# Kernel optimization log

Hardware: AMD Instinct MI355X
Metric: run time of the kernel (lower is better)

The kernel has to match this reference:

```python
import jax, jax.numpy as jnp
import numpy as np


def avg_pool_2x2(x):
    # x: [B, H, W, C] -> [B, H//2, W//2, C], non-overlapping 2x2 mean (Keras AveragePooling2D default)
    B, H, W, C = x.shape
    return x.reshape(B, H // 2, 2, W // 2, 2, C).mean(axis=(2, 4))


def setup_inputs() -> dict:
    key = jax.random.key(0)
    k1, k2, k3, k4, k5 = jax.random.split(key, 5)
    B, H, W, C = 16, 64, 64, 512
    x = jax.random.normal(k1, (B, H, W, C), dtype=jnp.float32)
    Wf = jax.random.normal(k2, (C, C // 8), dtype=jnp.float32) * 0.02
    Wg = jax.random.normal(k3, (C, C // 8), dtype=jnp.float32) * 0.02
    Wh = jax.random.normal(k4, (C, C // 2), dtype=jnp.float32) * 0.02
    Wo = jax.random.normal(k5, (C // 2, C), dtype=jnp.float32) * 0.02
    return {"x": x, "Wf": Wf, "Wg": Wg, "Wh": Wh, "Wo": Wo}


def reference(x, Wf, Wg, Wh, Wo):
    B, H, W, C = x.shape
    # 1x1 convs are per-pixel matmuls over channels
    f = jnp.einsum('bhwc,cd->bhwd', x, Wf).reshape(B, H * W, C // 8)          # queries
    xp = avg_pool_2x2(x)                                                      # [B,H/2,W/2,C]
    g = jnp.einsum('bhwc,cd->bhwd', xp, Wg).reshape(B, H * W // 4, C // 8)    # keys
    h = jnp.einsum('bhwc,cd->bhwd', xp, Wh).reshape(B, H * W // 4, C // 2)    # values
    attn = jax.nn.softmax(jnp.einsum('bqd,bkd->bqk', f, g), axis=-1)          # [B, HW, HW/4]
    y = jnp.einsum('bqk,bkd->bqd', attn, h).reshape(B, H, W, C // 2)
    out = jnp.einsum('bhwd,dc->bhwc', y, Wo) + x                              # residual
    return out
```

## Files before the change

### kernel.cpp

```cpp
#include <hip/hip_runtime.h>


#define DEVI static __device__ __forceinline__

typedef float f32x4  __attribute__((ext_vector_type(4)));
typedef float f32x16 __attribute__((ext_vector_type(16)));
typedef short bf16x8 __attribute__((ext_vector_type(8)));

DEVI short f2bf(float f) {
  union { float f; unsigned u; } v; v.f = f;
  unsigned r = v.u + 0x7FFFu + ((v.u >> 16) & 1u);
  return (short)(r >> 16);
}
DEVI float b2f(short s) {
  union { unsigned u; float f; } v; v.u = ((unsigned)(unsigned short)s) << 16; return v.f;
}
DEVI unsigned pack2(float a, float b) {
  return (unsigned)(unsigned short)f2bf(a) | ((unsigned)(unsigned short)f2bf(b) << 16);
}
DEVI f32x4 mfma16(bf16x8 a, bf16x8 b, f32x4 c) {
  return __builtin_amdgcn_mfma_f32_16x16x32_bf16(a, b, c, 0, 0, 0);
}
DEVI f32x16 mfma32(bf16x8 a, bf16x8 b, f32x16 c) {
  return __builtin_amdgcn_mfma_f32_32x32x16_bf16(a, b, c, 0, 0, 0);
}
DEVI void gload16(const short* gsrc, short* lds) {
  __builtin_amdgcn_global_load_lds(
      (const __attribute__((address_space(1))) void*)gsrc,
      (__attribute__((address_space(3))) void*)lds, 16, 0, 0);
}

__global__ __launch_bounds__(256) void prep_weights(
    const float* __restrict__ Wf, const float* __restrict__ Wg,
    const float* __restrict__ Wh, const float* __restrict__ Wo,
    short* __restrict__ WfT, short* __restrict__ WgT,
    short* __restrict__ WhT, short* __restrict__ WoT) {
  int i = blockIdx.x * 256 + threadIdx.x;
  const float* src; short* dst; int K, N, e;
  if (i < 32768)       { src = Wf; dst = WfT; K = 512; N = 64;  e = i; }
  else if (i < 65536)  { src = Wg; dst = WgT; K = 512; N = 64;  e = i - 32768; }
  else if (i < 196608) { src = Wh; dst = WhT; K = 512; N = 256; e = i - 65536; }
  else                 { src = Wo; dst = WoT; K = 256; N = 512; e = i - 196608; }
  int n = e / K, k = e - n * K;
  dst[e] = f2bf(src[(long)k * N + n]);
}

template<bool SRC_F32>
DEVI void stage64(short* lds, const void* gsrc, int rows, int stride, int tid) {
  const int chunks = rows * 8;
  for (int c = tid; c < chunks; c += 256) {
    int row = c >> 3, slot = c & 7;
    int dstb = row*128 + ((slot ^ (row & 7)) << 4);
    bf16x8 v;
    if (SRC_F32) {
      const float* s = (const float*)gsrc + (long)row*stride + slot*8;
      float4 u0 = *(const float4*)s;
      float4 u1 = *(const float4*)(s + 4);
      v[0]=f2bf(u0.x); v[1]=f2bf(u0.y); v[2]=f2bf(u0.z); v[3]=f2bf(u0.w);
      v[4]=f2bf(u1.x); v[5]=f2bf(u1.y); v[6]=f2bf(u1.z); v[7]=f2bf(u1.w);
    } else {
      v = *(const bf16x8*)((const short*)gsrc + (long)row*stride + slot*8);
    }
    *(bf16x8*)((char*)lds + dstb) = v;
  }
}

template<bool A_F32, bool POOL>
__global__ __launch_bounds__(256) void gemm_k512(const void* __restrict__ A,
    const short* __restrict__ BT, short* __restrict__ C, int Nfull,
    short* __restrict__ xp) {
  __shared__ short As[128*64];
  __shared__ short Bs[64*64];
  const int m0 = blockIdx.x * 128;
  const int n0 = blockIdx.y * 64;
  const int tid = threadIdx.x, w = tid >> 6, lane = tid & 63;
  const int l15 = lane & 15, lhi = lane >> 4;
  const int wr = w >> 1, wc = w & 1;
  f32x4 acc[4][2] = {};
  for (int kt = 0; kt < 8; ++kt) {
    const int k0 = kt * 64;
    if constexpr (A_F32)
      stage64<true >(As, (const float*)A + (long)m0*512 + k0, 128, 512, tid);
    else
      stage64<false>(As, (const short*)A + (long)m0*512 + k0, 128, 512, tid);
    stage64<false>(Bs, BT + (long)n0*512 + k0, 64, 512, tid);
    __syncthreads();
    if constexpr (POOL) {
      const long pr0 = (long)(m0 >> 12)*1024 + ((m0 & 4095) >> 7)*32;
      int wp = tid >> 3, cs = tid & 7;
      const char* Ab = (const char*)As;
      bf16x8 v00 = *(const bf16x8*)(Ab + (2*wp  )*128 + ((cs ^ ((2*wp  )&7))<<4));
      bf16x8 v01 = *(const bf16x8*)(Ab + (2*wp+1)*128 + ((cs ^ ((2*wp+1)&7))<<4));
      bf16x8 v10 = *(const bf16x8*)(Ab + (64+2*wp)*128 + ((cs ^ ((2*wp  )&7))<<4));
      bf16x8 v11 = *(const bf16x8*)(Ab + (65+2*wp)*128 + ((cs ^ ((2*wp+1)&7))<<4));
      bf16x8 o;
      #pragma unroll
      for (int j = 0; j < 8; ++j)
        o[j] = f2bf(0.25f*(b2f(v00[j])+b2f(v01[j])+b2f(v10[j])+b2f(v11[j])));
      *(bf16x8*)(xp + (pr0 + wp)*512 + k0 + cs*8) = o;
    }
    bf16x8 af[4][2], bfr[2][2];
    #pragma unroll
    for (int mi = 0; mi < 4; ++mi)
      #pragma unroll
      for (int ks = 0; ks < 2; ++ks) {
        int m = wr*64 + mi*16 + l15;
        int slot = lhi + ks*4;
        af[mi][ks] = *(const bf16x8*)((const char*)As + m*128 + ((slot ^ (m & 7)) << 4));
      }
    #pragma unroll
    for (int ni = 0; ni < 2; ++ni)
      #pragma unroll
      for (int ks = 0; ks < 2; ++ks) {
        int n = wc*32 + ni*16 + l15;
        int slot = lhi + ks*4;
        bfr[ni][ks] = *(const bf16x8*)((const char*)Bs + n*128 + ((slot ^ (n & 7)) << 4));
      }
    #pragma unroll
    for (int ks = 0; ks < 2; ++ks)
      #pragma unroll
      for (int mi = 0; mi < 4; ++mi)
        #pragma unroll
        for (int ni = 0; ni < 2; ++ni)
          acc[mi][ni] = mfma16(af[mi][ks], bfr[ni][ks], acc[mi][ni]);
    __syncthreads();
  }
  #pragma unroll
  for (int mi = 0; mi < 4; ++mi)
    #pragma unroll
    for (int ni = 0; ni < 2; ++ni)
      #pragma unroll
      for (int r = 0; r < 4; ++r) {
        long row = m0 + wr*64 + mi*16 + lhi*4 + r;
        int col = n0 + wc*32 + ni*16 + l15;
        C[row * (long)Nfull + col] = f2bf(acc[mi][ni][r]);
      }
}

__global__ __launch_bounds__(256) void transpose_h(const short* __restrict__ h,
                                                   short* __restrict__ hT) {
  __shared__ short t[64][72];
  const int k0 = blockIdx.x * 64, n0 = blockIdx.y * 64, b = blockIdx.z;
  const int tid = threadIdx.x;
  {
    int row = tid >> 2, cch = (tid & 3) * 16;
    const short* src = h + ((long)b*1024 + k0 + row) * 256 + n0 + cch;
    *(bf16x8*)&t[row][cch]     = *(const bf16x8*)src;
    *(bf16x8*)&t[row][cch + 8] = *(const bf16x8*)(src + 8);
  }
  __syncthreads();
  {
    int n = tid >> 2, kch = (tid & 3) * 16;
    bf16x8 lo, hi;
    #pragma unroll
    for (int j = 0; j < 8; ++j) { lo[j] = t[kch + j][n]; hi[j] = t[kch + 8 + j][n]; }
    short* dst = hT + ((long)b*256 + n0 + n) * 1024 + k0 + kch;
    *(bf16x8*)dst       = lo;
    *(bf16x8*)(dst + 8) = hi;
  }
}

__global__ __launch_bounds__(512, 2) void attn_kernel(const short* __restrict__ f,
    const short* __restrict__ g, const short* __restrict__ hT,
    const short* __restrict__ WoT, const float* __restrict__ x,
    float* __restrict__ out) {
  extern __shared__ __align__(16) char smem[];
  const int b = blockIdx.y, q0 = blockIdx.x * 256;
  const int tid = threadIdx.x, w = tid >> 6, lane = tid & 63;
  const int l31 = lane & 31, hi = lane >> 5;

  short* Pw = (short*)(smem + 81920 + w*4096);

  bf16x8 fq[4];
  {
    const short* frow = f + ((long)b*4096 + q0 + w*32 + l31) * 64;
    #pragma unroll
    for (int ks = 0; ks < 4; ++ks) fq[ks] = *(const bf16x8*)(frow + ks*16 + hi*8);
  }

  f32x16 acc2[8] = {};
  float rsq = 0.f;

  auto stage = [&](int buf, int kt) {
    const int k0 = kt * 64;
    short* gbuf = (short*)(smem + buf*8192);
    short* hbuf = (short*)(smem + 16384 + buf*32768);
    {
      int row = (w << 3) + (lane >> 3);
      int gslot = (lane & 7) ^ (row & 7);
      gload16(g + ((long)b*1024 + k0 + row)*64 + gslot*8, gbuf + w*512);
    }
    #pragma unroll
    for (int cc = 0; cc < 4; ++cc) {
      int c = (w << 2) + cc;
      int row = (c << 3) + (lane >> 3);
      int gslot = (lane & 7) ^ (row & 7);
      gload16(hT + ((long)b*256 + row)*1024 + k0 + gslot*8, hbuf + c*512);
    }
  };

  stage(0, 0);
  __syncthreads();
  int cur = 0;
  for (int kt = 0; kt < 16; ++kt) {
    if (kt < 15) stage(cur ^ 1, kt + 1);
    const char* gcur = (const char*)(smem + cur*8192);
    const char* hcur = (const char*)(smem + 16384 + cur*32768);
    #pragma unroll
    for (int kc2 = 0; kc2 < 2; ++kc2) {
      f32x16 s2 = {};
      #pragma unroll
      for (int ks = 0; ks < 4; ++ks) {
        int key = kc2*32 + l31;
        bf16x8 gb = *(const bf16x8*)(gcur + key*128 + (((ks*2 + hi) ^ (l31 & 7)) << 4));
        s2 = mfma32(gb, fq[ks], s2);
      }
      #pragma unroll
      for (int g2 = 0; g2 < 4; ++g2) {
        float p0 = __expf(s2[g2*4+0]), p1 = __expf(s2[g2*4+1]);
        float p2 = __expf(s2[g2*4+2]), p3 = __expf(s2[g2*4+3]);
        rsq += (p0 + p1) + (p2 + p3);
        uint2 pk; pk.x = pack2(p0, p1); pk.y = pack2(p2, p3);
        int byteoff = l31*128 + ((((kc2*4 + g2) ^ (l31 & 7)) << 4) + hi*8);
        *(uint2*)((char*)Pw + byteoff) = pk;
      }
    }
    asm volatile("s_waitcnt lgkmcnt(0)" ::: "memory");
    __builtin_amdgcn_sched_barrier(0);
    __builtin_amdgcn_s_setprio(1);
    #pragma unroll
    for (int ks = 0; ks < 4; ++ks) {
      bf16x8 pa = *(const bf16x8*)((const char*)Pw + l31*128 + (((ks*2 + hi) ^ (l31 & 7)) << 4));
      #pragma unroll
      for (int nc2 = 0; nc2 < 8; ++nc2) {
        int n = nc2*32 + l31;
        bf16x8 hb = *(const bf16x8*)(hcur + n*128 + (((ks*2 + hi) ^ (l31 & 7)) << 4));
        acc2[nc2] = mfma32(hb, pa, acc2[nc2]);
      }
    }
    __builtin_amdgcn_s_setprio(0);
    __syncthreads();
    cur ^= 1;
  }
  rsq += __shfl_xor(rsq, 32);
  float ri = 1.f / rsq;
  bf16x8 yB[16];
  #pragma unroll
  for (int nc2 = 0; nc2 < 8; ++nc2) {
    #pragma unroll
    for (int fh = 0; fh < 2; ++fh) {
      const int G = fh*8;
      unsigned a0 = pack2(acc2[nc2][G+0]*ri, acc2[nc2][G+1]*ri);
      unsigned a1 = pack2(acc2[nc2][G+2]*ri, acc2[nc2][G+3]*ri);
      unsigned b0 = pack2(acc2[nc2][G+4]*ri, acc2[nc2][G+5]*ri);
      unsigned b1 = pack2(acc2[nc2][G+6]*ri, acc2[nc2][G+7]*ri);
      asm volatile("v_permlane32_swap_b32 %0, %1" : "+v"(b0), "+v"(a0));
      asm volatile("v_permlane32_swap_b32 %0, %1" : "+v"(b1), "+v"(a1));
      union { unsigned u[4]; bf16x8 v; } pk;
      pk.u[0] = a0; pk.u[1] = a1; pk.u[2] = b0; pk.u[3] = b1;
      yB[nc2*2 + fh] = pk.v;
    }
  }
  const long qrow = (long)b*4096 + q0 + w*32 + l31;
  const float* xrow = x + qrow*512;
  float* orow = out + qrow*512;
  for (int cc2 = 0; cc2 < 16; ++cc2) {
    f32x16 ao = {};
    #pragma unroll
    for (int ns = 0; ns < 16; ++ns) {
      bf16x8 wo = *(const bf16x8*)(WoT + (cc2*32 + l31)*256 + ns*16 + hi*8);
      ao = mfma32(wo, yB[ns], ao);
    }
    #pragma unroll
    for (int g2 = 0; g2 < 4; ++g2) {
      int c = cc2*32 + g2*8 + hi*4;
      float4 xv = *(const float4*)(xrow + c);
      float4 ov;
      ov.x = ao[g2*4+0] + xv.x;
      ov.y = ao[g2*4+1] + xv.y;
      ov.z = ao[g2*4+2] + xv.z;
      ov.w = ao[g2*4+3] + xv.w;
      *(float4*)(orow + c) = ov;
    }
  }
}

extern "C" void kernel_launch(void* const* d_in, const int* in_sizes, int n_in,
                              void* d_out, int out_size, void* d_ws, size_t ws_size,
                              hipStream_t stream) {
  const float* x  = (const float*)d_in[0];
  const float* Wf = (const float*)d_in[1];
  const float* Wg = (const float*)d_in[2];
  const float* Wh = (const float*)d_in[3];
  const float* Wo = (const float*)d_in[4];
  float* out = (float*)d_out;

  short* xp  = (short*)d_ws;
  short* fb  = xp  + (long)16*1024*512;
  short* gb  = fb  + (long)65536*64;
  short* hb  = gb  + (long)16384*64;
  short* hTb = hb  + (long)16384*256;
  short* WfT = hTb + (long)16*256*1024;
  short* WgT = WfT + 64*512;
  short* WhT = WgT + 64*512;
  short* WoT = WhT + 256*512;

  hipFuncSetAttribute((const void*)attn_kernel,
                      hipFuncAttributeMaxDynamicSharedMemorySize, 114688);

  prep_weights<<<1536, 256, 0, stream>>>(Wf, Wg, Wh, Wo, WfT, WgT, WhT, WoT);
  gemm_k512<true , true ><<<dim3(512, 1), 256, 0, stream>>>((const void*)x,  WfT, fb, 64,  xp);
  gemm_k512<false, false><<<dim3(128, 1), 256, 0, stream>>>((const void*)xp, WgT, gb, 64,  nullptr);
  gemm_k512<false, false><<<dim3(128, 4), 256, 0, stream>>>((const void*)xp, WhT, hb, 256, nullptr);
  transpose_h <<<dim3(16, 4, 16), 256, 0, stream>>>(hb, hTb);
  attn_kernel <<<dim3(16, 16), 512, 114688, stream>>>(fb, gb, hTb, WoT, x, out);
}
```

Measured before the change: 207.8 us.

## Keep softmax probabilities in registers via permlane swap, halve attention block size

The exponentiated scores are packed into bf16 and rearranged across lane halves with v_permlane32_swap. This builds the MFMA B operand directly in registers, so the per-wave LDS round trip and its waitcnt are gone. Blocks shrink to 256 threads covering 128 queries, so the grid doubles to 512 blocks and LDS per block drops to 80KB. The Wo projection splits into two independent accumulator chains to expose more MFMA parallelism. Each g/h tile is now shared by fewer waves, which raises redundant global-to-LDS traffic per query.

```diff
diff --git a/kernel.cpp b/kernel.cpp
--- a/kernel.cpp
+++ b/kernel.cpp
@@ -160,16 +160,14 @@
   }
 }
 
-__global__ __launch_bounds__(512, 2) void attn_kernel(const short* __restrict__ f,
+__global__ __launch_bounds__(256, 2) void attn_kernel(const short* __restrict__ f,
     const short* __restrict__ g, const short* __restrict__ hT,
     const short* __restrict__ WoT, const float* __restrict__ x,
     float* __restrict__ out) {
   extern __shared__ __align__(16) char smem[];
-  const int b = blockIdx.y, q0 = blockIdx.x * 256;
+  const int b = blockIdx.y, q0 = blockIdx.x * 128;
   const int tid = threadIdx.x, w = tid >> 6, lane = tid & 63;
   const int l31 = lane & 31, hi = lane >> 5;
-
-  short* Pw = (short*)(smem + 81920 + w*4096);
 
   bf16x8 fq[4];
   {
@@ -185,17 +183,17 @@
     const int k0 = kt * 64;
     short* gbuf = (short*)(smem + buf*8192);
     short* hbuf = (short*)(smem + 16384 + buf*32768);
-    {
-      int row = (w << 3) + (lane >> 3);
-      int gslot = (lane & 7) ^ (row & 7);
-      gload16(g + ((long)b*1024 + k0 + row)*64 + gslot*8, gbuf + w*512);
-    }
-    #pragma unroll
-    for (int cc = 0; cc < 4; ++cc) {
-      int c = (w << 2) + cc;
-      int row = (c << 3) + (lane >> 3);
-      int gslot = (lane & 7) ^ (row & 7);
-      gload16(hT + ((long)b*256 + row)*1024 + k0 + gslot*8, hbuf + c*512);
+    #pragma unroll
+    for (int it = 0; it < 2; ++it) {
+      int c = it*256 + w*64 + lane;
+      int row = c >> 3, gslot = (c & 7) ^ (row & 7);
+      gload16(g + ((long)b*1024 + k0 + row)*64 + gslot*8, gbuf + (it*256 + w*64)*8);
+    }
+    #pragma unroll
+    for (int it = 0; it < 8; ++it) {
+      int c = it*256 + w*64 + lane;
+      int row = c >> 3, gslot = (c & 7) ^ (row & 7);
+      gload16(hT + ((long)b*256 + row)*1024 + k0 + gslot*8, hbuf + (it*256 + w*64)*8);
     }
   };
 
@@ -206,6 +204,7 @@
     if (kt < 15) stage(cur ^ 1, kt + 1);
     const char* gcur = (const char*)(smem + cur*8192);
     const char* hcur = (const char*)(smem + 16384 + cur*32768);
+    bf16x8 pa[4];
     #pragma unroll
     for (int kc2 = 0; kc2 < 2; ++kc2) {
       f32x16 s2 = {};
@@ -216,26 +215,30 @@
         s2 = mfma32(gb, fq[ks], s2);
       }
       #pragma unroll
-      for (int g2 = 0; g2 < 4; ++g2) {
-        float p0 = __expf(s2[g2*4+0]), p1 = __expf(s2[g2*4+1]);
-        float p2 = __expf(s2[g2*4+2]), p3 = __expf(s2[g2*4+3]);
-        rsq += (p0 + p1) + (p2 + p3);
-        uint2 pk; pk.x = pack2(p0, p1); pk.y = pack2(p2, p3);
-        int byteoff = l31*128 + ((((kc2*4 + g2) ^ (l31 & 7)) << 4) + hi*8);
-        *(uint2*)((char*)Pw + byteoff) = pk;
-      }
-    }
-    asm volatile("s_waitcnt lgkmcnt(0)" ::: "memory");
-    __builtin_amdgcn_sched_barrier(0);
+      for (int fh = 0; fh < 2; ++fh) {
+        const int G = fh*8;
+        float e0 = __expf(s2[G+0]), e1 = __expf(s2[G+1]);
+        float e2 = __expf(s2[G+2]), e3 = __expf(s2[G+3]);
+        float e4 = __expf(s2[G+4]), e5 = __expf(s2[G+5]);
+        float e6 = __expf(s2[G+6]), e7 = __expf(s2[G+7]);
+        rsq += ((e0 + e1) + (e2 + e3)) + ((e4 + e5) + (e6 + e7));
+        unsigned a0 = pack2(e0, e1), a1 = pack2(e2, e3);
+        unsigned b0 = pack2(e4, e5), b1 = pack2(e6, e7);
+        asm volatile("v_permlane32_swap_b32 %0, %1" : "+v"(b0), "+v"(a0));
+        asm volatile("v_permlane32_swap_b32 %0, %1" : "+v"(b1), "+v"(a1));
+        union { unsigned u[4]; bf16x8 v; } pk;
+        pk.u[0] = a0; pk.u[1] = a1; pk.u[2] = b0; pk.u[3] = b1;
+        pa[kc2*2 + fh] = pk.v;
+      }
+    }
     __builtin_amdgcn_s_setprio(1);
     #pragma unroll
     for (int ks = 0; ks < 4; ++ks) {
-      bf16x8 pa = *(const bf16x8*)((const char*)Pw + l31*128 + (((ks*2 + hi) ^ (l31 & 7)) << 4));
       #pragma unroll
       for (int nc2 = 0; nc2 < 8; ++nc2) {
         int n = nc2*32 + l31;
         bf16x8 hb = *(const bf16x8*)(hcur + n*128 + (((ks*2 + hi) ^ (l31 & 7)) << 4));
-        acc2[nc2] = mfma32(hb, pa, acc2[nc2]);
+        acc2[nc2] = mfma32(hb, pa[ks], acc2[nc2]);
       }
     }
     __builtin_amdgcn_s_setprio(0);
@@ -265,21 +268,23 @@
   const float* xrow = x + qrow*512;
   float* orow = out + qrow*512;
   for (int cc2 = 0; cc2 < 16; ++cc2) {
-    f32x16 ao = {};
-    #pragma unroll
-    for (int ns = 0; ns < 16; ++ns) {
-      bf16x8 wo = *(const bf16x8*)(WoT + (cc2*32 + l31)*256 + ns*16 + hi*8);
-      ao = mfma32(wo, yB[ns], ao);
+    f32x16 ao0 = {}, ao1 = {};
+    #pragma unroll
+    for (int ns2 = 0; ns2 < 8; ++ns2) {
+      bf16x8 wo0 = *(const bf16x8*)(WoT + (cc2*32 + l31)*256 + (2*ns2  )*16 + hi*8);
+      bf16x8 wo1 = *(const bf16x8*)(WoT + (cc2*32 + l31)*256 + (2*ns2+1)*16 + hi*8);
+      ao0 = mfma32(wo0, yB[2*ns2  ], ao0);
+      ao1 = mfma32(wo1, yB[2*ns2+1], ao1);
     }
     #pragma unroll
     for (int g2 = 0; g2 < 4; ++g2) {
       int c = cc2*32 + g2*8 + hi*4;
       float4 xv = *(const float4*)(xrow + c);
       float4 ov;
-      ov.x = ao[g2*4+0] + xv.x;
-      ov.y = ao[g2*4+1] + xv.y;
-      ov.z = ao[g2*4+2] + xv.z;
-      ov.w = ao[g2*4+3] + xv.w;
+      ov.x = ao0[g2*4+0] + ao1[g2*4+0] + xv.x;
+      ov.y = ao0[g2*4+1] + ao1[g2*4+1] + xv.y;
+      ov.z = ao0[g2*4+2] + ao1[g2*4+2] + xv.z;
+      ov.w = ao0[g2*4+3] + ao1[g2*4+3] + xv.w;
       *(float4*)(orow + c) = ov;
     }
   }
@@ -306,12 +311,12 @@
   short* WoT = WhT + 256*512;
 
   hipFuncSetAttribute((const void*)attn_kernel,
-                      hipFuncAttributeMaxDynamicSharedMemorySize, 114688);
+                      hipFuncAttributeMaxDynamicSharedMemorySize, 81920);
 
   prep_weights<<<1536, 256, 0, stream>>>(Wf, Wg, Wh, Wo, WfT, WgT, WhT, WoT);
   gemm_k512<true , true ><<<dim3(512, 1), 256, 0, stream>>>((const void*)x,  WfT, fb, 64,  xp);
   gemm_k512<false, false><<<dim3(128, 1), 256, 0, stream>>>((const void*)xp, WgT, gb, 64,  nullptr);
   gemm_k512<false, false><<<dim3(128, 4), 256, 0, stream>>>((const void*)xp, WhT, hb, 256, nullptr);
   transpose_h <<<dim3(16, 4, 16), 256, 0, stream>>>(hb, hTb);
-  attn_kernel <<<dim3(16, 16), 512, 114688, stream>>>(fb, gb, hTb, WoT, x, out);
-}
+  attn_kernel <<<dim3(32, 16), 256, 81920, stream>>>(fb, gb, hTb, WoT, x, out);
+}
```

Result: no change. 204.0 us (-1.8%).
